# Performance work log

Hardware: AMD Instinct MI355X
Metric: run time of the kernel (lower is better)

## Reference

```python
import jax, jax.numpy as jnp
import numpy as np

N_QUBITS = 6
DIM = 2 ** N_QUBITS  # 64


def _b(t, nd):
    # broadcast a (B,) per-sample angle factor (or scalar) against a state slice of rank nd
    if jnp.ndim(t) == 0:
        return t
    return t.reshape((t.shape[0],) + (1,) * (nd - 1))


def _ry(state, theta, q):
    ax = q + 1
    s0 = jnp.take(state, 0, axis=ax)
    s1 = jnp.take(state, 1, axis=ax)
    h = theta * 0.5
    c = _b(jnp.cos(h), s0.ndim)
    s = _b(jnp.sin(h), s0.ndim)
    return jnp.stack([c * s0 - s * s1, s * s0 + c * s1], axis=ax)


def _rx(state, theta, q):
    ax = q + 1
    s0 = jnp.take(state, 0, axis=ax)
    s1 = jnp.take(state, 1, axis=ax)
    h = theta * 0.5
    c = _b(jnp.cos(h), s0.ndim)
    s = _b(jnp.sin(h), s0.ndim)
    return jnp.stack([c * s0 - 1j * s * s1, -1j * s * s0 + c * s1], axis=ax)


def _rz(state, theta, q):
    ax = q + 1
    s0 = jnp.take(state, 0, axis=ax)
    s1 = jnp.take(state, 1, axis=ax)
    h = theta * 0.5
    p0 = _b(jnp.exp(-1j * h), s0.ndim)
    p1 = _b(jnp.exp(1j * h), s0.ndim)
    return jnp.stack([p0 * s0, p1 * s1], axis=ax)


def _cnot(state, ctrl, tgt):
    ca = ctrl + 1
    s0 = jnp.take(state, 0, axis=ca)
    s1 = jnp.take(state, 1, axis=ca)
    ta = tgt + 1 if tgt < ctrl else tgt  # target axis after removing control axis
    s1 = jnp.flip(s1, axis=ta)
    return jnp.stack([s0, s1], axis=ca)


def quantum_circuit(inputs, weights):
    # inputs: (B, 6) float; weights: (5, 6) float -> (B, 6) PauliZ expectations
    B = inputs.shape[0]
    scaled = jnp.clip(inputs, -1.0, 1.0) * jnp.pi
    state = jnp.zeros((B,) + (2,) * N_QUBITS, dtype=jnp.complex64)
    state = state.at[(slice(None),) + (0,) * N_QUBITS].set(1.0)
    for i in range(N_QUBITS):
        state = _ry(state, scaled[:, i], i)
    for i in range(N_QUBITS):
        state = _rx(state, weights[0, i], i)
        state = _rz(state, weights[1, i], i)
    for i in range(N_QUBITS - 1):
        state = _cnot(state, i, i + 1)
    state = _cnot(state, N_QUBITS - 1, 0)
    for i in range(N_QUBITS):
        state = _ry(state, weights[2, i], i)
        state = _rz(state, weights[3, i], i)
    for i in range(0, N_QUBITS, 2):
        state = _cnot(state, i, (i + 1) % N_QUBITS)
    for i in range(N_QUBITS):
        state = _rx(state, weights[4, i], i)
    probs = (state.real ** 2 + state.imag ** 2).reshape(B, DIM)
    # Z eigenvalue table: qubit q is bit (5-q) of the flat index
    k = jnp.arange(DIM)
    z = (1 - 2 * ((k[None, :] >> (N_QUBITS - 1 - jnp.arange(N_QUBITS)[:, None])) & 1)).astype(jnp.float32)
    return probs @ z.T  # (B, 6)


def setup_inputs() -> dict:
    key = jax.random.key(0)
    ks = jax.random.split(key, 13)
    B, n_symptoms, n_dep, nq = 262144, 128, 20, N_QUBITS

    def lin(k, fi, fo):
        bound = 1.0 / np.sqrt(fi)
        kw, kb = jax.random.split(k)
        W = jax.random.uniform(kw, (fi, fo), jnp.float32, -bound, bound)
        b = jax.random.uniform(kb, (fo,), jnp.float32, -bound, bound)
        return W, b

    x = jax.random.normal(ks[0], (B, n_symptoms), jnp.float32)
    W1, b1 = lin(ks[1], n_symptoms, 32)
    W2, b2 = lin(ks[2], 32, 16)
    W3, b3 = lin(ks[3], 16, nq)
    qw = jax.random.normal(ks[4], (5, nq), jnp.float32)
    W4, b4 = lin(ks[5], nq, 16)
    W5, b5 = lin(ks[6], 16, n_dep)
    return {"x": x, "W1": W1, "b1": b1, "W2": W2, "b2": b2, "W3": W3, "b3": b3,
            "qw": qw, "W4": W4, "b4": b4, "W5": W5, "b5": b5}


def reference(x, W1, b1, W2, b2, W3, b3, qw, W4, b4, W5, b5):
    h = jax.nn.relu(x @ W1 + b1)            # Dropout(0.2) is identity at eval
    h = jax.nn.relu(h @ W2 + b2)
    pre = jnp.tanh(h @ W3 + b3)             # (B, 6)
    # Original detaches before the quantum circuit -> stop_gradient for fidelity
    q_out = quantum_circuit(jax.lax.stop_gradient(pre), jax.lax.stop_gradient(qw))
    h = jax.nn.relu(q_out @ W4 + b4)
    return h @ W5 + b5                      # (B, n_departments)
```

## Files before the change

kernel.cpp:

```cpp
#include <hip/hip_runtime.h>
#include <hip/hip_bf16.h>
#include <math.h>

#define PI_F 3.14159265358979323846f

typedef float f32x4 __attribute__((ext_vector_type(4)));
typedef short bf16x8 __attribute__((ext_vector_type(8)));

__device__ __forceinline__ unsigned short bf_hi(float f) {
    return (unsigned short)(__float_as_uint(f) >> 16);
}
__device__ __forceinline__ float from_bf(unsigned short h) {
    return __uint_as_float(((unsigned)h) << 16);
}

__global__ __launch_bounds__(64) void build_u(const float* __restrict__ qw,
                                              float* __restrict__ Umat) {
    const int l = threadIdx.x;
    const int b = blockIdx.x;

    float ar = (l == b) ? 1.0f : 0.0f;
    float ai = 0.0f;

    #pragma unroll
    for (int i = 0; i < 6; ++i) {
        const int mask = 1 << (5 - i);
        float th = 0.5f * qw[0 * 6 + i];
        float c = cosf(th), sn = sinf(th);
        float pr = __shfl_xor(ar, mask);
        float pi = __shfl_xor(ai, mask);
        float nr = c * ar + sn * pi;
        float ni = c * ai - sn * pr;
        ar = nr; ai = ni;
        th = 0.5f * qw[1 * 6 + i];
        c = cosf(th); sn = sinf(th);
        float zn = (l & mask) ? 1.0f : -1.0f;
        nr = c * ar - zn * sn * ai;
        ni = c * ai + zn * sn * ar;
        ar = nr; ai = ni;
    }

    #pragma unroll
    for (int i = 0; i < 6; ++i) {
        const int ctrl = i, tgt = (i + 1) % 6;
        const int cm = 1 << (5 - ctrl), tm = 1 << (5 - tgt);
        float pr = __shfl_xor(ar, tm);
        float pi = __shfl_xor(ai, tm);
        bool take = (l & cm) != 0;
        ar = take ? pr : ar;
        ai = take ? pi : ai;
    }

    #pragma unroll
    for (int i = 0; i < 6; ++i) {
        const int mask = 1 << (5 - i);
        float th = 0.5f * qw[2 * 6 + i];
        float c = cosf(th), sn = sinf(th);
        float pr = __shfl_xor(ar, mask);
        float pi = __shfl_xor(ai, mask);
        float sg = (l & mask) ? sn : -sn;
        float nr = c * ar + sg * pr;
        float ni = c * ai + sg * pi;
        ar = nr; ai = ni;
        th = 0.5f * qw[3 * 6 + i];
        c = cosf(th); sn = sinf(th);
        float zn = (l & mask) ? 1.0f : -1.0f;
        nr = c * ar - zn * sn * ai;
        ni = c * ai + zn * sn * ar;
        ar = nr; ai = ni;
    }

    #pragma unroll
    for (int i = 0; i < 6; i += 2) {
        const int cm = 1 << (5 - i), tm = 1 << (5 - (i + 1));
        float pr = __shfl_xor(ar, tm);
        float pi = __shfl_xor(ai, tm);
        bool take = (l & cm) != 0;
        ar = take ? pr : ar;
        ai = take ? pi : ai;
    }

    #pragma unroll
    for (int i = 0; i < 6; ++i) {
        const int mask = 1 << (5 - i);
        float th = 0.5f * qw[4 * 6 + i];
        float c = cosf(th), sn = sinf(th);
        float pr = __shfl_xor(ar, mask);
        float pi = __shfl_xor(ai, mask);
        float nr = c * ar + sn * pi;
        float ni = c * ai - sn * pr;
        ar = nr; ai = ni;
    }

    Umat[(l * 64 + b) * 2 + 0] = ar;
    Umat[(l * 64 + b) * 2 + 1] = ai;
}

__global__ __launch_bounds__(64) void convert_all(
    const float* __restrict__ Umat, const float* __restrict__ W1,
    unsigned short* __restrict__ Ubf, unsigned short* __restrict__ W1bf)
{
    const int l = threadIdx.x;
    bf16x8* out8 = reinterpret_cast<bf16x8*>(Ubf);

    #pragma unroll
    for (int ri = 0; ri < 2; ++ri) {
        #pragma unroll
        for (int t = 0; t < 4; ++t) {
            #pragma unroll
            for (int h = 0; h < 2; ++h) {
                const int vf = (ri * 4 + t) * 2 + h;
                bf16x8 vh, vl;
                #pragma unroll
                for (int e = 0; e < 8; ++e) {
                    const int k = 16 * t + (l & 15);
                    const int j = h * 32 + (l >> 4) * 8 + e;
                    float v = Umat[k * 128 + j * 2 + ri];
                    unsigned short hh = bf_hi(v);
                    vh[e] = (short)hh;
                    vl[e] = (short)bf_hi(v - from_bf(hh));
                }
                out8[(vf * 2 + 0) * 64 + l] = vh;
                out8[(vf * 2 + 1) * 64 + l] = vl;
            }
        }
    }

    bf16x8* w8 = reinterpret_cast<bf16x8*>(W1bf);
    #pragma unroll
    for (int ks = 0; ks < 4; ++ks) {
        #pragma unroll
        for (int nt = 0; nt < 2; ++nt) {
            bf16x8 vh, vl;
            #pragma unroll
            for (int e = 0; e < 8; ++e) {
                float v = W1[(ks * 32 + (l >> 4) * 8 + e) * 32 + nt * 16 + (l & 15)];
                unsigned short hh = bf_hi(v);
                vh[e] = (short)hh;
                vl[e] = (short)bf_hi(v - from_bf(hh));
            }
            w8[((ks * 2 + nt) * 2 + 0) * 64 + l] = vh;
            w8[((ks * 2 + nt) * 2 + 1) * 64 + l] = vl;
        }
    }
}

__device__ __forceinline__ void front_tail(
    const float h1[32],
    const float* __restrict__ W2, const float* __restrict__ b2,
    const float* __restrict__ W3, const float* __restrict__ b3,
    float lo[8], float hi[8])
{
    float h2[16];
    #pragma unroll
    for (int o = 0; o < 16; ++o) h2[o] = b2[o];
    #pragma unroll
    for (int j = 0; j < 32; ++j) {
        #pragma unroll
        for (int o = 0; o < 16; ++o) h2[o] = fmaf(h1[j], W2[j * 16 + o], h2[o]);
    }
    #pragma unroll
    for (int o = 0; o < 16; ++o) h2[o] = fmaxf(h2[o], 0.0f);

    float cq[6], sq[6];
    #pragma unroll
    for (int q = 0; q < 6; ++q) {
        float t = b3[q];
        #pragma unroll
        for (int j = 0; j < 16; ++j) t = fmaf(h2[j], W3[j * 6 + q], t);
        t = tanhf(t);
        t = fminf(1.0f, fmaxf(-1.0f, t));
        float half = t * (0.5f * PI_F);
        sq[q] = sinf(half);
        cq[q] = cosf(half);
    }

    {
        float f3[2] = {cq[3], sq[3]};
        float f4[2] = {cq[4], sq[4]};
        float f5[2] = {cq[5], sq[5]};
        #pragma unroll
        for (int m = 0; m < 8; ++m)
            lo[m] = f3[(m >> 2) & 1] * f4[(m >> 1) & 1] * f5[m & 1];
        float f0[2] = {cq[0], sq[0]};
        float f1[2] = {cq[1], sq[1]};
        float f2[2] = {cq[2], sq[2]};
        #pragma unroll
        for (int m = 0; m < 8; ++m)
            hi[m] = f0[(m >> 2) & 1] * f1[(m >> 1) & 1] * f2[m & 1];
    }
}

__global__ __launch_bounds__(256) void front_mfma(
    const float* __restrict__ x,
    const unsigned short* __restrict__ W1bf, const float* __restrict__ b1,
    const float* __restrict__ W2, const float* __restrict__ b2,
    const float* __restrict__ W3, const float* __restrict__ b3,
    float* __restrict__ tab, int B)
{
    __shared__ float smem[256 * 36];

    const int tid  = threadIdx.x;
    const int wv   = tid >> 6;
    const int lane = tid & 63;
    const int g    = lane >> 4;
    const int c    = lane & 15;
    const long blk = (long)blockIdx.x * 256;

    const f32x4* xg = reinterpret_cast<const f32x4*>(x);
    const bf16x8* Wb = reinterpret_cast<const bf16x8*>(W1bf);

    f32x4 acc0[4], acc1[4];
    #pragma unroll
    for (int mt = 0; mt < 4; ++mt) { acc0[mt] = (f32x4)0.0f; acc1[mt] = (f32x4)0.0f; }

    #pragma unroll 1
    for (int ks = 0; ks < 4; ++ks) {
        #pragma unroll
        for (int i = 0; i < 8; ++i) {
            const int flat = i * 256 + tid;
            const int row = flat >> 3;
            const int c4  = flat & 7;
            long srow = blk + row;
            if (srow >= B) srow = B - 1;
            f32x4 v = __builtin_nontemporal_load(&xg[(size_t)srow * 32 + ks * 8 + c4]);
            *reinterpret_cast<f32x4*>(&smem[row * 36 + c4 * 4]) = v;
        }
        __syncthreads();

        bf16x8 B0h = Wb[((ks * 2 + 0) * 2 + 0) * 64 + lane];
        bf16x8 B0l = Wb[((ks * 2 + 0) * 2 + 1) * 64 + lane];
        bf16x8 B1h = Wb[((ks * 2 + 1) * 2 + 0) * 64 + lane];
        bf16x8 B1l = Wb[((ks * 2 + 1) * 2 + 1) * 64 + lane];

        #pragma unroll
        for (int mt = 0; mt < 4; ++mt) {
            const int row = wv * 64 + mt * 16 + c;
            f32x4 xa = *reinterpret_cast<const f32x4*>(&smem[row * 36 + g * 8]);
            f32x4 xb = *reinterpret_cast<const f32x4*>(&smem[row * 36 + g * 8 + 4]);

            bf16x8 Ah, Al;
            #pragma unroll
            for (int e = 0; e < 4; ++e) {
                unsigned short hh = bf_hi(xa[e]);
                Ah[e] = (short)hh;
                Al[e] = (short)bf_hi(xa[e] - from_bf(hh));
            }
            #pragma unroll
            for (int e = 0; e < 4; ++e) {
                unsigned short hh = bf_hi(xb[e]);
                Ah[4 + e] = (short)hh;
                Al[4 + e] = (short)bf_hi(xb[e] - from_bf(hh));
            }

            acc0[mt] = __builtin_amdgcn_mfma_f32_16x16x32_bf16(Ah, B0h, acc0[mt], 0, 0, 0);
            acc0[mt] = __builtin_amdgcn_mfma_f32_16x16x32_bf16(Al, B0h, acc0[mt], 0, 0, 0);
            acc0[mt] = __builtin_amdgcn_mfma_f32_16x16x32_bf16(Ah, B0l, acc0[mt], 0, 0, 0);
            acc1[mt] = __builtin_amdgcn_mfma_f32_16x16x32_bf16(Ah, B1h, acc1[mt], 0, 0, 0);
            acc1[mt] = __builtin_amdgcn_mfma_f32_16x16x32_bf16(Al, B1h, acc1[mt], 0, 0, 0);
            acc1[mt] = __builtin_amdgcn_mfma_f32_16x16x32_bf16(Ah, B1l, acc1[mt], 0, 0, 0);
        }
        __syncthreads();
    }

    #pragma unroll
    for (int mt = 0; mt < 4; ++mt) {
        #pragma unroll
        for (int r = 0; r < 4; ++r) {
            smem[(wv * 64 + mt * 16 + g * 4 + r) * 33 + c]      = acc0[mt][r];
            smem[(wv * 64 + mt * 16 + g * 4 + r) * 33 + 16 + c] = acc1[mt][r];
        }
    }

    __syncthreads();

    const int s = (int)(blk + tid);
    float h1[32];
    #pragma unroll
    for (int o = 0; o < 32; ++o) h1[o] = fmaxf(smem[tid * 33 + o] + b1[o], 0.0f);

    float lo[8], hi[8];
    front_tail(h1, W2, b2, W3, b3, lo, hi);

    if (s < B) {
        #pragma unroll
        for (int i = 0; i < 8; ++i)
            __builtin_nontemporal_store(lo[i], &tab[(size_t)i * B + s]);
        #pragma unroll
        for (int i = 0; i < 8; ++i)
            __builtin_nontemporal_store(hi[i], &tab[(size_t)(8 + i) * B + s]);
    }
}

__global__ __launch_bounds__(256) void gemv_mfma(
    const float* __restrict__ tab,
    const unsigned short* __restrict__ Ubf,
    const float* __restrict__ W4, const float* __restrict__ b4,
    const float* __restrict__ W5, const float* __restrict__ b5,
    float* __restrict__ out, int B)
{
    __shared__ float qlds[64][8];

    const int tid  = threadIdx.x;
    const int wv   = tid >> 6;
    const int lane = tid & 63;
    const int g    = lane >> 4;
    const int c    = lane & 15;
    const long blk = (long)blockIdx.x * 64;
    const int s    = (int)(blk + wv * 16 + c);
    const int s_ld = (s < B) ? s : (B - 1);

    float tl[8], th[8];
    #pragma unroll
    for (int i = 0; i < 8; ++i)
        tl[i] = __builtin_nontemporal_load(&tab[(size_t)i * B + s_ld]);
    #pragma unroll
    for (int i = 0; i < 8; ++i)
        th[i] = __builtin_nontemporal_load(&tab[(size_t)(8 + i) * B + s_ld]);

    float bh0 = (g == 0) ? th[0] : (g == 1) ? th[1] : (g == 2) ? th[2] : th[3];
    float bh1 = (g == 0) ? th[4] : (g == 1) ? th[5] : (g == 2) ? th[6] : th[7];

    bf16x8 Ah0, Al0, Ah1, Al1;
    #pragma unroll
    for (int e = 0; e < 8; ++e) {
        float p0 = bh0 * tl[e];
        unsigned short h0 = bf_hi(p0);
        Ah0[e] = (short)h0;
        Al0[e] = (short)bf_hi(p0 - from_bf(h0));
        float p1 = bh1 * tl[e];
        unsigned short h1 = bf_hi(p1);
        Ah1[e] = (short)h1;
        Al1[e] = (short)bf_hi(p1 - from_bf(h1));
    }

    const bf16x8* Ub = reinterpret_cast<const bf16x8*>(Ubf);

    f32x4 accre[4], accim[4];
    #pragma unroll
    for (int t = 0; t < 4; ++t) { accre[t] = (f32x4)0.0f; accim[t] = (f32x4)0.0f; }

    #pragma unroll
    for (int t = 0; t < 4; ++t) {
        bf16x8 B0h = Ub[(((0 * 4 + t) * 2 + 0) * 2 + 0) * 64 + lane];
        bf16x8 B0l = Ub[(((0 * 4 + t) * 2 + 0) * 2 + 1) * 64 + lane];
        bf16x8 B1h = Ub[(((0 * 4 + t) * 2 + 1) * 2 + 0) * 64 + lane];
        bf16x8 B1l = Ub[(((0 * 4 + t) * 2 + 1) * 2 + 1) * 64 + lane];
        accre[t] = __builtin_amdgcn_mfma_f32_16x16x32_bf16(Ah0, B0h, accre[t], 0, 0, 0);
        accre[t] = __builtin_amdgcn_mfma_f32_16x16x32_bf16(Al0, B0h, accre[t], 0, 0, 0);
        accre[t] = __builtin_amdgcn_mfma_f32_16x16x32_bf16(Ah0, B0l, accre[t], 0, 0, 0);
        accre[t] = __builtin_amdgcn_mfma_f32_16x16x32_bf16(Ah1, B1h, accre[t], 0, 0, 0);
        accre[t] = __builtin_amdgcn_mfma_f32_16x16x32_bf16(Al1, B1h, accre[t], 0, 0, 0);
        accre[t] = __builtin_amdgcn_mfma_f32_16x16x32_bf16(Ah1, B1l, accre[t], 0, 0, 0);
    }
    #pragma unroll
    for (int t = 0; t < 4; ++t) {
        bf16x8 B0h = Ub[(((1 * 4 + t) * 2 + 0) * 2 + 0) * 64 + lane];
        bf16x8 B0l = Ub[(((1 * 4 + t) * 2 + 0) * 2 + 1) * 64 + lane];
        bf16x8 B1h = Ub[(((1 * 4 + t) * 2 + 1) * 2 + 0) * 64 + lane];
        bf16x8 B1l = Ub[(((1 * 4 + t) * 2 + 1) * 2 + 1) * 64 + lane];
        accim[t] = __builtin_amdgcn_mfma_f32_16x16x32_bf16(Ah0, B0h, accim[t], 0, 0, 0);
        accim[t] = __builtin_amdgcn_mfma_f32_16x16x32_bf16(Al0, B0h, accim[t], 0, 0, 0);
        accim[t] = __builtin_amdgcn_mfma_f32_16x16x32_bf16(Ah0, B0l, accim[t], 0, 0, 0);
        accim[t] = __builtin_amdgcn_mfma_f32_16x16x32_bf16(Ah1, B1h, accim[t], 0, 0, 0);
        accim[t] = __builtin_amdgcn_mfma_f32_16x16x32_bf16(Al1, B1h, accim[t], 0, 0, 0);
        accim[t] = __builtin_amdgcn_mfma_f32_16x16x32_bf16(Ah1, B1l, accim[t], 0, 0, 0);
    }

    #pragma unroll
    for (int r = 0; r < 4; ++r) {
        float p0 = accre[0][r] * accre[0][r] + accim[0][r] * accim[0][r];
        float p1 = accre[1][r] * accre[1][r] + accim[1][r] * accim[1][r];
        float p2 = accre[2][r] * accre[2][r] + accim[2][r] * accim[2][r];
        float p3 = accre[3][r] * accre[3][r] + accim[3][r] * accim[3][r];

        float P0 = p0 + p1 + p2 + p3;
        float P1 = p0 + p1 - p2 - p3;
        float P2 = p0 - p1 + p2 - p3;

        float v = P0;
        #pragma unroll
        for (int st = 0; st < 4; ++st) {
            const int m = 1 << st;
            float prt = __shfl_xor(v, m);
            v = (lane & m) ? (prt - v) : (prt + v);
        }
        #pragma unroll
        for (int st = 0; st < 4; ++st) P1 += __shfl_xor(P1, 1 << st);
        #pragma unroll
        for (int st = 0; st < 4; ++st) P2 += __shfl_xor(P2, 1 << st);

        const int sl = wv * 16 + g * 4 + r;
        if (c == 0) { qlds[sl][0] = P1; qlds[sl][1] = P2; }
        if (c == 8) qlds[sl][2] = v;
        if (c == 4) qlds[sl][3] = v;
        if (c == 2) qlds[sl][4] = v;
        if (c == 1) qlds[sl][5] = v;
    }

    __syncthreads();

    if (tid < 64) {
        const int so = (int)(blk + tid);
        if (so < B) {
            float qv[6];
            #pragma unroll
            for (int i = 0; i < 6; ++i) qv[i] = qlds[tid][i];

            float h4[16];
            #pragma unroll
            for (int o = 0; o < 16; ++o) h4[o] = b4[o];
            #pragma unroll
            for (int q = 0; q < 6; ++q) {
                #pragma unroll
                for (int o = 0; o < 16; ++o) h4[o] = fmaf(qv[q], W4[q * 16 + o], h4[o]);
            }
            #pragma unroll
            for (int o = 0; o < 16; ++o) h4[o] = fmaxf(h4[o], 0.0f);

            float o5[20];
            #pragma unroll
            for (int o = 0; o < 20; ++o) {
                float t = b5[o];
                #pragma unroll
                for (int j = 0; j < 16; ++j) t = fmaf(h4[j], W5[j * 20 + o], t);
                o5[o] = t;
            }

            f32x4* outv = reinterpret_cast<f32x4*>(out + (size_t)so * 20);
            #pragma unroll
            for (int i = 0; i < 5; ++i) {
                f32x4 v = {o5[4 * i], o5[4 * i + 1], o5[4 * i + 2], o5[4 * i + 3]};
                __builtin_nontemporal_store(v, &outv[i]);
            }
        }
    }
}

extern "C" void kernel_launch(void* const* d_in, const int* in_sizes, int n_in,
                              void* d_out, int out_size, void* d_ws, size_t ws_size,
                              hipStream_t stream) {
    const float* x  = (const float*)d_in[0];
    const float* W1 = (const float*)d_in[1];
    const float* b1 = (const float*)d_in[2];
    const float* W2 = (const float*)d_in[3];
    const float* b2 = (const float*)d_in[4];
    const float* W3 = (const float*)d_in[5];
    const float* b3 = (const float*)d_in[6];
    const float* qw = (const float*)d_in[7];
    const float* W4 = (const float*)d_in[8];
    const float* b4 = (const float*)d_in[9];
    const float* W5 = (const float*)d_in[10];
    const float* b5 = (const float*)d_in[11];
    float* out = (float*)d_out;

    const int B = in_sizes[0] / 128;

    float* Umat = (float*)d_ws;
    unsigned short* Ubf  = (unsigned short*)((float*)d_ws + 8192);
    unsigned short* W1bf = (unsigned short*)((float*)d_ws + 16384);
    float* tab  = (float*)d_ws + 20480;

    build_u<<<64, 64, 0, stream>>>(qw, Umat);
    convert_all<<<1, 64, 0, stream>>>(Umat, W1, Ubf, W1bf);
    front_mfma<<<(B + 255) / 256, 256, 0, stream>>>(
        x, W1bf, b1, W2, b2, W3, b3, tab, B);
    gemv_mfma<<<(B + 63) / 64, 256, 0, stream>>>(
        tab, Ubf, W4, b4, W5, b5, out, B);
}
```

Measured before the change: 97.46 us.

## Merge unitary build and bf16 conversion into one kernel; widen gemv blocks

```diff
diff --git a/kernel.cpp b/kernel.cpp
--- a/kernel.cpp
+++ b/kernel.cpp
@@ -14,134 +14,136 @@
     return __uint_as_float(((unsigned)h) << 16);
 }
 
-__global__ __launch_bounds__(64) void build_u(const float* __restrict__ qw,
-                                              float* __restrict__ Umat) {
-    const int l = threadIdx.x;
-    const int b = blockIdx.x;
-
-    float ar = (l == b) ? 1.0f : 0.0f;
-    float ai = 0.0f;
-
-    #pragma unroll
-    for (int i = 0; i < 6; ++i) {
-        const int mask = 1 << (5 - i);
-        float th = 0.5f * qw[0 * 6 + i];
-        float c = cosf(th), sn = sinf(th);
-        float pr = __shfl_xor(ar, mask);
-        float pi = __shfl_xor(ai, mask);
-        float nr = c * ar + sn * pi;
-        float ni = c * ai - sn * pr;
-        ar = nr; ai = ni;
-        th = 0.5f * qw[1 * 6 + i];
-        c = cosf(th); sn = sinf(th);
-        float zn = (l & mask) ? 1.0f : -1.0f;
-        nr = c * ar - zn * sn * ai;
-        ni = c * ai + zn * sn * ar;
-        ar = nr; ai = ni;
-    }
-
-    #pragma unroll
-    for (int i = 0; i < 6; ++i) {
-        const int ctrl = i, tgt = (i + 1) % 6;
-        const int cm = 1 << (5 - ctrl), tm = 1 << (5 - tgt);
-        float pr = __shfl_xor(ar, tm);
-        float pi = __shfl_xor(ai, tm);
-        bool take = (l & cm) != 0;
-        ar = take ? pr : ar;
-        ai = take ? pi : ai;
-    }
-
-    #pragma unroll
-    for (int i = 0; i < 6; ++i) {
-        const int mask = 1 << (5 - i);
-        float th = 0.5f * qw[2 * 6 + i];
-        float c = cosf(th), sn = sinf(th);
-        float pr = __shfl_xor(ar, mask);
-        float pi = __shfl_xor(ai, mask);
-        float sg = (l & mask) ? sn : -sn;
-        float nr = c * ar + sg * pr;
-        float ni = c * ai + sg * pi;
-        ar = nr; ai = ni;
-        th = 0.5f * qw[3 * 6 + i];
-        c = cosf(th); sn = sinf(th);
-        float zn = (l & mask) ? 1.0f : -1.0f;
-        nr = c * ar - zn * sn * ai;
-        ni = c * ai + zn * sn * ar;
-        ar = nr; ai = ni;
-    }
-
-    #pragma unroll
-    for (int i = 0; i < 6; i += 2) {
-        const int cm = 1 << (5 - i), tm = 1 << (5 - (i + 1));
-        float pr = __shfl_xor(ar, tm);
-        float pi = __shfl_xor(ai, tm);
-        bool take = (l & cm) != 0;
-        ar = take ? pr : ar;
-        ai = take ? pi : ai;
-    }
-
-    #pragma unroll
-    for (int i = 0; i < 6; ++i) {
-        const int mask = 1 << (5 - i);
-        float th = 0.5f * qw[4 * 6 + i];
-        float c = cosf(th), sn = sinf(th);
-        float pr = __shfl_xor(ar, mask);
-        float pi = __shfl_xor(ai, mask);
-        float nr = c * ar + sn * pi;
-        float ni = c * ai - sn * pr;
-        ar = nr; ai = ni;
-    }
-
-    Umat[(l * 64 + b) * 2 + 0] = ar;
-    Umat[(l * 64 + b) * 2 + 1] = ai;
-}
-
-__global__ __launch_bounds__(64) void convert_all(
-    const float* __restrict__ Umat, const float* __restrict__ W1,
+__global__ __launch_bounds__(256) void prep(
+    const float* __restrict__ qw, const float* __restrict__ W1,
     unsigned short* __restrict__ Ubf, unsigned short* __restrict__ W1bf)
 {
-    const int l = threadIdx.x;
+    __shared__ float Us[8192];
+
+    const int tid = threadIdx.x;
+    const int wv  = tid >> 6;
+    const int l   = tid & 63;
+
+    #pragma unroll 1
+    for (int i = 0; i < 16; ++i) {
+        const int b = wv * 16 + i;
+
+        float ar = (l == b) ? 1.0f : 0.0f;
+        float ai = 0.0f;
+
+        #pragma unroll
+        for (int q = 0; q < 6; ++q) {
+            const int mask = 1 << (5 - q);
+            float th = 0.5f * qw[0 * 6 + q];
+            float c = cosf(th), sn = sinf(th);
+            float pr = __shfl_xor(ar, mask);
+            float pi = __shfl_xor(ai, mask);
+            float nr = c * ar + sn * pi;
+            float ni = c * ai - sn * pr;
+            ar = nr; ai = ni;
+            th = 0.5f * qw[1 * 6 + q];
+            c = cosf(th); sn = sinf(th);
+            float zn = (l & mask) ? 1.0f : -1.0f;
+            nr = c * ar - zn * sn * ai;
+            ni = c * ai + zn * sn * ar;
+            ar = nr; ai = ni;
+        }
+
+        #pragma unroll
+        for (int q = 0; q < 6; ++q) {
+            const int ctrl = q, tgt = (q + 1) % 6;
+            const int cm = 1 << (5 - ctrl), tm = 1 << (5 - tgt);
+            float pr = __shfl_xor(ar, tm);
+            float pi = __shfl_xor(ai, tm);
+            bool take = (l & cm) != 0;
+            ar = take ? pr : ar;
+            ai = take ? pi : ai;
+        }
+
+        #pragma unroll
+        for (int q = 0; q < 6; ++q) {
+            const int mask = 1 << (5 - q);
+            float th = 0.5f * qw[2 * 6 + q];
+            float c = cosf(th), sn = sinf(th);
+            float pr = __shfl_xor(ar, mask);
+            float pi = __shfl_xor(ai, mask);
+            float sg = (l & mask) ? sn : -sn;
+            float nr = c * ar + sg * pr;
+            float ni = c * ai + sg * pi;
+            ar = nr; ai = ni;
+            th = 0.5f * qw[3 * 6 + q];
+            c = cosf(th); sn = sinf(th);
+            float zn = (l & mask) ? 1.0f : -1.0f;
+            nr = c * ar - zn * sn * ai;
+            ni = c * ai + zn * sn * ar;
+            ar = nr; ai = ni;
+        }
+
+        #pragma unroll
+        for (int q = 0; q < 6; q += 2) {
+            const int cm = 1 << (5 - q), tm = 1 << (5 - (q + 1));
+            float pr = __shfl_xor(ar, tm);
+            float pi = __shfl_xor(ai, tm);
+            bool take = (l & cm) != 0;
+            ar = take ? pr : ar;
+            ai = take ? pi : ai;
+        }
+
+        #pragma unroll
+        for (int q = 0; q < 6; ++q) {
+            const int mask = 1 << (5 - q);
+            float th = 0.5f * qw[4 * 6 + q];
+            float c = cosf(th), sn = sinf(th);
+            float pr = __shfl_xor(ar, mask);
+            float pi = __shfl_xor(ai, mask);
+            float nr = c * ar + sn * pi;
+            float ni = c * ai - sn * pr;
+            ar = nr; ai = ni;
+        }
+
+        Us[(l * 64 + b) * 2 + 0] = ar;
+        Us[(l * 64 + b) * 2 + 1] = ai;
+    }
+
+    __syncthreads();
+
     bf16x8* out8 = reinterpret_cast<bf16x8*>(Ubf);
-
-    #pragma unroll
-    for (int ri = 0; ri < 2; ++ri) {
-        #pragma unroll
-        for (int t = 0; t < 4; ++t) {
-            #pragma unroll
-            for (int h = 0; h < 2; ++h) {
-                const int vf = (ri * 4 + t) * 2 + h;
-                bf16x8 vh, vl;
-                #pragma unroll
-                for (int e = 0; e < 8; ++e) {
-                    const int k = 16 * t + (l & 15);
-                    const int j = h * 32 + (l >> 4) * 8 + e;
-                    float v = Umat[k * 128 + j * 2 + ri];
-                    unsigned short hh = bf_hi(v);
-                    vh[e] = (short)hh;
-                    vl[e] = (short)bf_hi(v - from_bf(hh));
-                }
-                out8[(vf * 2 + 0) * 64 + l] = vh;
-                out8[(vf * 2 + 1) * 64 + l] = vl;
-            }
-        }
+    #pragma unroll
+    for (int q = 0; q < 4; ++q) {
+        const int vf = wv * 4 + q;
+        const int h  = vf & 1;
+        const int tt = (vf >> 1) & 3;
+        const int ri = vf >> 3;
+        bf16x8 vh, vl;
+        #pragma unroll
+        for (int e = 0; e < 8; ++e) {
+            const int k = 16 * tt + (l & 15);
+            const int j = h * 32 + (l >> 4) * 8 + e;
+            float v = Us[(k * 64 + j) * 2 + ri];
+            unsigned short hh = bf_hi(v);
+            vh[e] = (short)hh;
+            vl[e] = (short)bf_hi(v - from_bf(hh));
+        }
+        out8[(vf * 2 + 0) * 64 + l] = vh;
+        out8[(vf * 2 + 1) * 64 + l] = vl;
     }
 
     bf16x8* w8 = reinterpret_cast<bf16x8*>(W1bf);
     #pragma unroll
-    for (int ks = 0; ks < 4; ++ks) {
-        #pragma unroll
-        for (int nt = 0; nt < 2; ++nt) {
-            bf16x8 vh, vl;
-            #pragma unroll
-            for (int e = 0; e < 8; ++e) {
-                float v = W1[(ks * 32 + (l >> 4) * 8 + e) * 32 + nt * 16 + (l & 15)];
-                unsigned short hh = bf_hi(v);
-                vh[e] = (short)hh;
-                vl[e] = (short)bf_hi(v - from_bf(hh));
-            }
-            w8[((ks * 2 + nt) * 2 + 0) * 64 + l] = vh;
-            w8[((ks * 2 + nt) * 2 + 1) * 64 + l] = vl;
-        }
+    for (int q = 0; q < 2; ++q) {
+        const int kombo = wv * 2 + q;
+        const int ks = kombo >> 1;
+        const int nt = kombo & 1;
+        bf16x8 vh, vl;
+        #pragma unroll
+        for (int e = 0; e < 8; ++e) {
+            float v = W1[(ks * 32 + (l >> 4) * 8 + e) * 32 + nt * 16 + (l & 15)];
+            unsigned short hh = bf_hi(v);
+            vh[e] = (short)hh;
+            vl[e] = (short)bf_hi(v - from_bf(hh));
+        }
+        w8[(kombo * 2 + 0) * 64 + l] = vh;
+        w8[(kombo * 2 + 1) * 64 + l] = vl;
     }
 }
 
@@ -299,134 +301,140 @@
     const float* __restrict__ W5, const float* __restrict__ b5,
     float* __restrict__ out, int B)
 {
-    __shared__ float qlds[64][8];
+    __shared__ float qlds[256 * 9];
 
     const int tid  = threadIdx.x;
     const int wv   = tid >> 6;
     const int lane = tid & 63;
     const int g    = lane >> 4;
     const int c    = lane & 15;
-    const long blk = (long)blockIdx.x * 64;
-    const int s    = (int)(blk + wv * 16 + c);
-    const int s_ld = (s < B) ? s : (B - 1);
-
-    float tl[8], th[8];
-    #pragma unroll
-    for (int i = 0; i < 8; ++i)
-        tl[i] = __builtin_nontemporal_load(&tab[(size_t)i * B + s_ld]);
-    #pragma unroll
-    for (int i = 0; i < 8; ++i)
-        th[i] = __builtin_nontemporal_load(&tab[(size_t)(8 + i) * B + s_ld]);
-
-    float bh0 = (g == 0) ? th[0] : (g == 1) ? th[1] : (g == 2) ? th[2] : th[3];
-    float bh1 = (g == 0) ? th[4] : (g == 1) ? th[5] : (g == 2) ? th[6] : th[7];
-
-    bf16x8 Ah0, Al0, Ah1, Al1;
-    #pragma unroll
-    for (int e = 0; e < 8; ++e) {
-        float p0 = bh0 * tl[e];
-        unsigned short h0 = bf_hi(p0);
-        Ah0[e] = (short)h0;
-        Al0[e] = (short)bf_hi(p0 - from_bf(h0));
-        float p1 = bh1 * tl[e];
-        unsigned short h1 = bf_hi(p1);
-        Ah1[e] = (short)h1;
-        Al1[e] = (short)bf_hi(p1 - from_bf(h1));
-    }
+    const long blk = (long)blockIdx.x * 256;
 
     const bf16x8* Ub = reinterpret_cast<const bf16x8*>(Ubf);
 
-    f32x4 accre[4], accim[4];
-    #pragma unroll
-    for (int t = 0; t < 4; ++t) { accre[t] = (f32x4)0.0f; accim[t] = (f32x4)0.0f; }
-
-    #pragma unroll
-    for (int t = 0; t < 4; ++t) {
-        bf16x8 B0h = Ub[(((0 * 4 + t) * 2 + 0) * 2 + 0) * 64 + lane];
-        bf16x8 B0l = Ub[(((0 * 4 + t) * 2 + 0) * 2 + 1) * 64 + lane];
-        bf16x8 B1h = Ub[(((0 * 4 + t) * 2 + 1) * 2 + 0) * 64 + lane];
-        bf16x8 B1l = Ub[(((0 * 4 + t) * 2 + 1) * 2 + 1) * 64 + lane];
-        accre[t] = __builtin_amdgcn_mfma_f32_16x16x32_bf16(Ah0, B0h, accre[t], 0, 0, 0);
-        accre[t] = __builtin_amdgcn_mfma_f32_16x16x32_bf16(Al0, B0h, accre[t], 0, 0, 0);
-        accre[t] = __builtin_amdgcn_mfma_f32_16x16x32_bf16(Ah0, B0l, accre[t], 0, 0, 0);
-        accre[t] = __builtin_amdgcn_mfma_f32_16x16x32_bf16(Ah1, B1h, accre[t], 0, 0, 0);
-        accre[t] = __builtin_amdgcn_mfma_f32_16x16x32_bf16(Al1, B1h, accre[t], 0, 0, 0);
-        accre[t] = __builtin_amdgcn_mfma_f32_16x16x32_bf16(Ah1, B1l, accre[t], 0, 0, 0);
-    }
-    #pragma unroll
-    for (int t = 0; t < 4; ++t) {
-        bf16x8 B0h = Ub[(((1 * 4 + t) * 2 + 0) * 2 + 0) * 64 + lane];
-        bf16x8 B0l = Ub[(((1 * 4 + t) * 2 + 0) * 2 + 1) * 64 + lane];
-        bf16x8 B1h = Ub[(((1 * 4 + t) * 2 + 1) * 2 + 0) * 64 + lane];
-        bf16x8 B1l = Ub[(((1 * 4 + t) * 2 + 1) * 2 + 1) * 64 + lane];
-        accim[t] = __builtin_amdgcn_mfma_f32_16x16x32_bf16(Ah0, B0h, accim[t], 0, 0, 0);
-        accim[t] = __builtin_amdgcn_mfma_f32_16x16x32_bf16(Al0, B0h, accim[t], 0, 0, 0);
-        accim[t] = __builtin_amdgcn_mfma_f32_16x16x32_bf16(Ah0, B0l, accim[t], 0, 0, 0);
-        accim[t] = __builtin_amdgcn_mfma_f32_16x16x32_bf16(Ah1, B1h, accim[t], 0, 0, 0);
-        accim[t] = __builtin_amdgcn_mfma_f32_16x16x32_bf16(Al1, B1h, accim[t], 0, 0, 0);
-        accim[t] = __builtin_amdgcn_mfma_f32_16x16x32_bf16(Ah1, B1l, accim[t], 0, 0, 0);
-    }
-
-    #pragma unroll
-    for (int r = 0; r < 4; ++r) {
-        float p0 = accre[0][r] * accre[0][r] + accim[0][r] * accim[0][r];
-        float p1 = accre[1][r] * accre[1][r] + accim[1][r] * accim[1][r];
-        float p2 = accre[2][r] * accre[2][r] + accim[2][r] * accim[2][r];
-        float p3 = accre[3][r] * accre[3][r] + accim[3][r] * accim[3][r];
-
-        float P0 = p0 + p1 + p2 + p3;
-        float P1 = p0 + p1 - p2 - p3;
-        float P2 = p0 - p1 + p2 - p3;
-
-        float v = P0;
-        #pragma unroll
-        for (int st = 0; st < 4; ++st) {
-            const int m = 1 << st;
-            float prt = __shfl_xor(v, m);
-            v = (lane & m) ? (prt - v) : (prt + v);
-        }
-        #pragma unroll
-        for (int st = 0; st < 4; ++st) P1 += __shfl_xor(P1, 1 << st);
-        #pragma unroll
-        for (int st = 0; st < 4; ++st) P2 += __shfl_xor(P2, 1 << st);
-
-        const int sl = wv * 16 + g * 4 + r;
-        if (c == 0) { qlds[sl][0] = P1; qlds[sl][1] = P2; }
-        if (c == 8) qlds[sl][2] = v;
-        if (c == 4) qlds[sl][3] = v;
-        if (c == 2) qlds[sl][4] = v;
-        if (c == 1) qlds[sl][5] = v;
+    #pragma unroll 1
+    for (int mt = 0; mt < 4; ++mt) {
+        const int s    = (int)(blk + wv * 64 + mt * 16 + c);
+        const int s_ld = (s < B) ? s : (B - 1);
+
+        float tl[8], th[8];
+        #pragma unroll
+        for (int i = 0; i < 8; ++i)
+            tl[i] = __builtin_nontemporal_load(&tab[(size_t)i * B + s_ld]);
+        #pragma unroll
+        for (int i = 0; i < 8; ++i)
+            th[i] = __builtin_nontemporal_load(&tab[(size_t)(8 + i) * B + s_ld]);
+
+        float bh0 = (g == 0) ? th[0] : (g == 1) ? th[1] : (g == 2) ? th[2] : th[3];
+        float bh1 = (g == 0) ? th[4] : (g == 1) ? th[5] : (g == 2) ? th[6] : th[7];
+
+        bf16x8 Ah0, Al0, Ah1, Al1;
+        #pragma unroll
+        for (int e = 0; e < 8; ++e) {
+            float p0 = bh0 * tl[e];
+            unsigned short h0 = bf_hi(p0);
+            Ah0[e] = (short)h0;
+            Al0[e] = (short)bf_hi(p0 - from_bf(h0));
+            float p1 = bh1 * tl[e];
+            unsigned short h1 = bf_hi(p1);
+            Ah1[e] = (short)h1;
+            Al1[e] = (short)bf_hi(p1 - from_bf(h1));
+        }
+
+        f32x4 accre[4], accim[4];
+        #pragma unroll
+        for (int t = 0; t < 4; ++t) { accre[t] = (f32x4)0.0f; accim[t] = (f32x4)0.0f; }
+
+        #pragma unroll
+        for (int t = 0; t < 4; ++t) {
+            bf16x8 B0h = Ub[(((0 * 4 + t) * 2 + 0) * 2 + 0) * 64 + lane];
+            bf16x8 B0l = Ub[(((0 * 4 + t) * 2 + 0) * 2 + 1) * 64 + lane];
+            bf16x8 B1h = Ub[(((0 * 4 + t) * 2 + 1) * 2 + 0) * 64 + lane];
+            bf16x8 B1l = Ub[(((0 * 4 + t) * 2 + 1) * 2 + 1) * 64 + lane];
+            accre[t] = __builtin_amdgcn_mfma_f32_16x16x32_bf16(Ah0, B0h, accre[t], 0, 0, 0);
+            accre[t] = __builtin_amdgcn_mfma_f32_16x16x32_bf16(Al0, B0h, accre[t], 0, 0, 0);
+            accre[t] = __builtin_amdgcn_mfma_f32_16x16x32_bf16(Ah0, B0l, accre[t], 0, 0, 0);
+            accre[t] = __builtin_amdgcn_mfma_f32_16x16x32_bf16(Ah1, B1h, accre[t], 0, 0, 0);
+            accre[t] = __builtin_amdgcn_mfma_f32_16x16x32_bf16(Al1, B1h, accre[t], 0, 0, 0);
+            accre[t] = __builtin_amdgcn_mfma_f32_16x16x32_bf16(Ah1, B1l, accre[t], 0, 0, 0);
+        }
+        #pragma unroll
+        for (int t = 0; t < 4; ++t) {
+            bf16x8 B0h = Ub[(((1 * 4 + t) * 2 + 0) * 2 + 0) * 64 + lane];
+            bf16x8 B0l = Ub[(((1 * 4 + t) * 2 + 0) * 2 + 1) * 64 + lane];
+            bf16x8 B1h = Ub[(((1 * 4 + t) * 2 + 1) * 2 + 0) * 64 + lane];
+            bf16x8 B1l = Ub[(((1 * 4 + t) * 2 + 1) * 2 + 1) * 64 + lane];
+            accim[t] = __builtin_amdgcn_mfma_f32_16x16x32_bf16(Ah0, B0h, accim[t], 0, 0, 0);
+            accim[t] = __builtin_amdgcn_mfma_f32_16x16x32_bf16(Al0, B0h, accim[t], 0, 0, 0);
+            accim[t] = __builtin_amdgcn_mfma_f32_16x16x32_bf16(Ah0, B0l, accim[t], 0, 0, 0);
+            accim[t] = __builtin_amdgcn_mfma_f32_16x16x32_bf16(Ah1, B1h, accim[t], 0, 0, 0);
+            accim[t] = __builtin_amdgcn_mfma_f32_16x16x32_bf16(Al1, B1h, accim[t], 0, 0, 0);
+            accim[t] = __builtin_amdgcn_mfma_f32_16x16x32_bf16(Ah1, B1l, accim[t], 0, 0, 0);
+        }
+
+        #pragma unroll
+        for (int r = 0; r < 4; ++r) {
+            float p0 = accre[0][r] * accre[0][r] + accim[0][r] * accim[0][r];
+            float p1 = accre[1][r] * accre[1][r] + accim[1][r] * accim[1][r];
+            float p2 = accre[2][r] * accre[2][r] + accim[2][r] * accim[2][r];
+            float p3 = accre[3][r] * accre[3][r] + accim[3][r] * accim[3][r];
+
+            float P0 = p0 + p1 + p2 + p3;
+            float P1 = p0 + p1 - p2 - p3;
+            float P2 = p0 - p1 + p2 - p3;
+
+            float v = P0;
+            #pragma unroll
+            for (int st = 0; st < 4; ++st) {
+                const int m = 1 << st;
+                float prt = __shfl_xor(v, m);
+                v = (lane & m) ? (prt - v) : (prt + v);
+            }
+            #pragma unroll
+            for (int st = 0; st < 4; ++st) P1 += __shfl_xor(P1, 1 << st);
+            #pragma unroll
+            for (int st = 0; st < 4; ++st) P2 += __shfl_xor(P2, 1 << st);
+
+            const int so = wv * 64 + mt * 16 + g * 4 + r;
+            float* qrow = &qlds[so * 9];
+            if (c == 0) { qrow[0] = P1; qrow[1] = P2; }
+            if (c == 8) qrow[2] = v;
+            if (c == 4) qrow[3] = v;
+            if (c == 2) qrow[4] = v;
+            if (c == 1) qrow[5] = v;
+        }
     }
 
     __syncthreads();
 
-    if (tid < 64) {
+    {
         const int so = (int)(blk + tid);
+        const float* qrow = &qlds[tid * 9];
+        float qv[6];
+        #pragma unroll
+        for (int i = 0; i < 6; ++i) qv[i] = qrow[i];
+
+        float h4[16];
+        #pragma unroll
+        for (int o = 0; o < 16; ++o) h4[o] = b4[o];
+        #pragma unroll
+        for (int q = 0; q < 6; ++q) {
+            #pragma unroll
+            for (int o = 0; o < 16; ++o) h4[o] = fmaf(qv[q], W4[q * 16 + o], h4[o]);
+        }
+        #pragma unroll
+        for (int o = 0; o < 16; ++o) h4[o] = fmaxf(h4[o], 0.0f);
+
+        float o5[20];
+        #pragma unroll
+        for (int o = 0; o < 20; ++o) {
+            float t = b5[o];
+            #pragma unroll
+            for (int j = 0; j < 16; ++j) t = fmaf(h4[j], W5[j * 20 + o], t);
+            o5[o] = t;
+        }
+
         if (so < B) {
-            float qv[6];
-            #pragma unroll
-            for (int i = 0; i < 6; ++i) qv[i] = qlds[tid][i];
-
-            float h4[16];
-            #pragma unroll
-            for (int o = 0; o < 16; ++o) h4[o] = b4[o];
-            #pragma unroll
-            for (int q = 0; q < 6; ++q) {
-                #pragma unroll
-                for (int o = 0; o < 16; ++o) h4[o] = fmaf(qv[q], W4[q * 16 + o], h4[o]);
-            }
-            #pragma unroll
-            for (int o = 0; o < 16; ++o) h4[o] = fmaxf(h4[o], 0.0f);
-
-            float o5[20];
-            #pragma unroll
-            for (int o = 0; o < 20; ++o) {
-                float t = b5[o];
-                #pragma unroll
-                for (int j = 0; j < 16; ++j) t = fmaf(h4[j], W5[j * 20 + o], t);
-                o5[o] = t;
-            }
-
             f32x4* outv = reinterpret_cast<f32x4*>(out + (size_t)so * 20);
             #pragma unroll
             for (int i = 0; i < 5; ++i) {
@@ -456,15 +464,13 @@
 
     const int B = in_sizes[0] / 128;
 
-    float* Umat = (float*)d_ws;
-    unsigned short* Ubf  = (unsigned short*)((float*)d_ws + 8192);
-    unsigned short* W1bf = (unsigned short*)((float*)d_ws + 16384);
-    float* tab  = (float*)d_ws + 20480;
-
-    build_u<<<64, 64, 0, stream>>>(qw, Umat);
-    convert_all<<<1, 64, 0, stream>>>(Umat, W1, Ubf, W1bf);
+    unsigned short* Ubf  = (unsigned short*)d_ws;
+    unsigned short* W1bf = Ubf + 16384;
+    float* tab = (float*)(W1bf + 8192);
+
+    prep<<<1, 256, 0, stream>>>(qw, W1, Ubf, W1bf);
     front_mfma<<<(B + 255) / 256, 256, 0, stream>>>(
         x, W1bf, b1, W2, b2, W3, b3, tab, B);
-    gemv_mfma<<<(B + 63) / 64, 256, 0, stream>>>(
+    gemv_mfma<<<(B + 255) / 256, 256, 0, stream>>>(
         tab, Ubf, W4, b4, W5, b5, out, B);
 }
```

Result: slower. 126.7 us (+30.0%).
